# Kernel tuning notes

Hardware: AMD Instinct MI355X
Metric: run time of the kernel (lower is better)

Reference implementation:

```python
import jax, jax.numpy as jnp
import numpy as np

B, L, M = 8, 200, 4
S, D, Q = 100, 128, 10000
NRG = NPC = NAC = 20
F = 4                       # len(forget_window)+1
NTOT = F * (NRG + NPC + NAC + 15)   # 300


def setup_inputs():
    key = jax.random.key(0)
    ks = jax.random.split(key, 40)
    ri = lambda k, sh, hi: jax.random.randint(k, sh, 0, hi)
    rn = lambda k, sh: jax.random.normal(k, sh, jnp.float32) * 0.02

    def make_c(k1, k2):
        # distinct concept ids per (b,l) row (matches typical data; makes scatter deterministic)
        base = jax.random.randint(k1, (B, L, 1), 0, S)
        cc = (base + jnp.arange(M)) % S
        mask = jax.random.uniform(k2, (B, L, M)) < 0.2
        return jnp.where(mask, -1, cc)

    inp = dict(
        q=ri(ks[0], (B, L), Q),
        c=make_c(ks[1], ks[2]),
        shift_q=ri(ks[3], (B, L), Q),
        shift_c=make_c(ks[4], ks[5]),
        r=ri(ks[6], (B, L), 2),
        rgaps=ri(ks[7], (B, L, M), NRG),
        pcounts=ri(ks[8], (B, L, M, F), NPC),
        acounts=ri(ks[9], (B, L, M, F), NAC),
        shft_rgaps=ri(ks[10], (B, L, M), NRG),
        shft_pcounts=ri(ks[11], (B, L, M, F), NPC),
        shft_acounts=ri(ks[12], (B, L, M, F), NAC),
        E_skill=rn(ks[13], (S, D)),
        E_question=rn(ks[14], (Q, D)),
        E_response=rn(ks[15], (2, D)),
        wih_in=rn(ks[16], (4 * D, D)), whh_in=rn(ks[17], (4 * D, D)),
        bih_in=rn(ks[18], (4 * D,)), bhh_in=rn(ks[19], (4 * D,)),
        wih_fg=rn(ks[20], (4 * D, D)), whh_fg=rn(ks[21], (4 * D, D)),
        bih_fg=rn(ks[22], (4 * D,)), bhh_fg=rn(ks[23], (4 * D,)),
        W_l2=rn(ks[24], (3 * D, D)), b_l2=rn(ks[25], (D,)),
        W_l3=rn(ks[26], (2 * D, D)), b_l3=rn(ks[27], (D,)),
        W_fc3=rn(ks[28], (2 * D, 1)), b_fc3=rn(ks[29], (1,)),
        W_fc4=rn(ks[30], (2 * D, D)), b_fc4=rn(ks[31], (D,)),
        W_fc5=rn(ks[32], (2 * D, D)), b_fc5=rn(ks[33], (D,)),
        W_cemb=rn(ks[34], (NTOT, D)),                      # cemb, no bias
        W_pre=rn(ks[35], (S * (D + NTOT), D)), b_pre=rn(ks[36], (D,)),
    )
    return inp


def _lstm(x, wih, whh, bih, bhh):
    # Faithful to source: torch LSTM default is seq-first and the module passes
    # [B,L,D] unchanged, so recurrence runs over axis 0 of the given tensor.
    H = whh.shape[1]

    def step(carry, xt):
        h, cs = carry
        g = xt @ wih.T + h @ whh.T + bih + bhh
        i, f, gg, o = jnp.split(g, 4, axis=-1)
        cs = jax.nn.sigmoid(f) * cs + jax.nn.sigmoid(i) * jnp.tanh(gg)
        h = jax.nn.sigmoid(o) * jnp.tanh(cs)
        return (h, cs), h

    z = jnp.zeros((x.shape[1], H), x.dtype)
    _, hs = jax.lax.scan(step, (z, z), x)
    return hs


def _concept_true(c, E_skill):
    # eye(S+1)[c][..., :-1] summed over M: -1 maps to an all-zero row
    cv1 = jax.nn.one_hot(c, S).sum(-2)              # [B,L,S]
    return cv1[..., None] * E_skill[None, None]     # [B,L,S,D]


def _attention(q, ct):
    scores = jnp.einsum('bld,blsd->bls', q, ct) / jnp.asarray(np.sqrt(D), q.dtype)
    w = jax.nn.softmax(scores, axis=-1)
    return jnp.einsum('bls,blsd->bld', w, ct)


def _forget(c, rg, pc, ac, E_skill, W_cemb, W_pre, b_pre):
    rg4 = jnp.broadcast_to(rg[..., None], (B, L, M, F))
    fv1 = jnp.concatenate([
        jax.nn.one_hot(rg4, NRG + 5).reshape(B, L, M, -1),
        jax.nn.one_hot(pc, NPC + 5).reshape(B, L, M, -1),
        jax.nn.one_hot(ac, NAC + 5).reshape(B, L, M, -1)], -1)   # [B,L,M,NTOT]
    # vectorized masked scatter replacing the triple Python loop: -1 -> dummy row S
    tgt = jnp.where(c < 0, S, c)
    bi = jnp.arange(B)[:, None, None]
    li = jnp.arange(L)[None, :, None]
    fv2 = jnp.zeros((B, L, S + 1, NTOT), fv1.dtype).at[bi, li, tgt].set(fv1)[:, :, :S]
    Cct = fv2 @ W_cemb                                           # [B,L,S,D]
    theta = _concept_true(c, E_skill) * Cct
    theta = jnp.concatenate([theta, fv2], -1).reshape(B, L, -1)  # [B,L,S*(D+NTOT)]
    return theta @ W_pre + b_pre


def reference(q, c, shift_q, shift_c, r, rgaps, pcounts, acounts,
              shft_rgaps, shft_pcounts, shft_acounts,
              E_skill, E_question, E_response,
              wih_in, whh_in, bih_in, bhh_in,
              wih_fg, whh_fg, bih_fg, bhh_fg,
              W_l2, b_l2, W_l3, b_l3, W_fc3, b_fc3,
              W_fc4, b_fc4, W_fc5, b_fc5, W_cemb, W_pre, b_pre):
    emb_q = E_question[q]
    emb_r = E_response[r]
    att = _attention(emb_q, _concept_true(c, E_skill))
    xemb = jnp.concatenate([emb_q, emb_r, att], -1) @ W_l2 + b_l2
    input_h = _lstm(xemb, wih_in, whh_in, bih_in, bhh_in)        # dropout = eval identity
    fh = _forget(c, rgaps, pcounts, acounts, E_skill, W_cemb, W_pre, b_pre)
    forget_h = _lstm(fh, wih_fg, whh_fg, bih_fg, bhh_fg)
    shift = E_question[shift_q]
    s_att = _attention(shift, _concept_true(shift_c, E_skill))
    shift = jnp.concatenate([shift, s_att], -1) @ W_l3 + b_l3
    shift_forget = _forget(shift_c, shft_rgaps, shft_pcounts, shft_acounts,
                           E_skill, W_cemb, W_pre, b_pre)
    x1 = jax.nn.relu(jnp.concatenate([shift, input_h], -1) @ W_fc4 + b_fc4)
    x2 = jax.nn.relu(jnp.concatenate([shift_forget, forget_h], -1) @ W_fc5 + b_fc5)
    y = jax.nn.sigmoid(jnp.concatenate([x1, x2], -1) @ W_fc3 + b_fc3)
    return y.squeeze(-1)   # [B,L]
```

## Files before the change

kernel.cpp:

```cpp
#include <hip/hip_runtime.h>
#include <hip/hip_bf16.h>
#include <math.h>

#define BB   8
#define LL   200
#define MM   4
#define SS   100
#define DD   128
#define FF   4
#define NT   300
#define ROWS (BB*LL)
#define JT   32

#define NB_TR  128
#define NB_TP  1000
#define NB_AT  800
#define NB_PJ  400
#define NB_FH  1600

__device__ __forceinline__ float sigf(float x){ return 1.f/(1.f+expf(-x)); }

__global__ void __launch_bounds__(256) k_stage1(
    const float* __restrict__ wih_in, const float* __restrict__ wih_fg,
    const float* __restrict__ whh_in, const float* __restrict__ whh_fg,
    float* __restrict__ wT_in, float* __restrict__ wT_fg,
    float* __restrict__ whhT_in, float* __restrict__ whhT_fg,
    const float* __restrict__ Es, const float* __restrict__ Wc,
    const float* __restrict__ Wp, float* __restrict__ T,
    const int* __restrict__ q,  const int* __restrict__ c,
    const int* __restrict__ sq, const int* __restrict__ sc,
    const float* __restrict__ Eq,
    float* __restrict__ att0, float* __restrict__ att1)
{
    __shared__ float WcL[JT][128];
    int b   = blockIdx.x;
    int tid = threadIdx.x;

    if (b < NB_TR) {
        for (int e = b*256 + tid; e < 4*65536; e += NB_TR*256) {
            int mat = e >> 16, o = e & 65535;
            int k = o >> 9, g = o & 511;
            const float* src = (mat==0)?wih_in:(mat==1)?wih_fg:(mat==2)?whh_in:whh_fg;
            float*       dst = (mat==0)?wT_in:(mat==1)?wT_fg:(mat==2)?whhT_in:whhT_fg;
            dst[o] = src[g*128 + k];
        }
        return;
    }
    if (b < NB_TR + NB_TP) {
        int bb2 = b - NB_TR;
        int s  = bb2 / 10;
        int jc = bb2 - s*10;
        int j0 = jc * JT;
        const float* es = Es + s*128;
        for (int idx = tid; idx < JT*128; idx += 256) {
            int jj = idx >> 7, d = idx & 127;
            int j = j0 + jj;
            WcL[jj][d] = (j < NT) ? Wc[j*128 + d] * es[d] : 0.f;
        }
        __syncthreads();

        const float*  wp  = Wp + (size_t)s*428*128;
        const float2* wp2 = (const float2*)wp;
        int tt = tid & 63;
        int jg = tid >> 6;
        float2 acc[8];
        #pragma unroll
        for (int u = 0; u < 8; u++) acc[u] = make_float2(0.f, 0.f);
        for (int db = 0; db < 128; db += 8) {
            float2 wb[8];
            #pragma unroll
            for (int u = 0; u < 8; u++) wb[u] = wp2[(db+u)*64 + tt];
            #pragma unroll
            for (int u = 0; u < 8; u++) {
                #pragma unroll
                for (int j = 0; j < 8; j++) {
                    float wc = WcL[jg*8 + j][db + u];
                    acc[j].x += wc * wb[u].x;
                    acc[j].y += wc * wb[u].y;
                }
            }
        }
        const float2* wpe = (const float2*)(wp + 128*128);
        float2* T2 = (float2*)T;
        #pragma unroll
        for (int u = 0; u < 8; u++) {
            int j = j0 + jg*8 + u;
            if (j < NT) {
                float2 bv = wpe[(size_t)j*64 + tt];
                float2 o; o.x = acc[u].x + bv.x; o.y = acc[u].y + bv.y;
                T2[((size_t)s*NT + j)*64 + tt] = o;
            }
        }
        return;
    }
    {
        int wv   = tid >> 6;
        int lane = tid & 63;
        int task = (b - NB_TR - NB_TP)*4 + wv;
        int row   = task >> 1;
        int which = task & 1;
        const int* qq = which ? sq : q;
        const int* cc = which ? sc : c;
        float* out = which ? att1 : att0;

        size_t qb = (size_t)qq[row]*128;
        float eq0 = Eq[qb + lane];
        float eq1 = Eq[qb + 64 + lane];
        int   s[4];
        float es0[4], es1[4], d[4];
        #pragma unroll
        for (int m = 0; m < 4; m++) {
            s[m]  = cc[row*4 + m];
            es0[m] = (s[m] >= 0) ? Es[s[m]*128 + lane]      : 0.f;
            es1[m] = (s[m] >= 0) ? Es[s[m]*128 + 64 + lane] : 0.f;
            d[m] = eq0*es0[m] + eq1*es1[m];
        }
        #pragma unroll
        for (int off = 32; off > 0; off >>= 1) {
            #pragma unroll
            for (int m = 0; m < 4; m++) d[m] += __shfl_xor(d[m], off);
        }
        const float inv = 0.08838834764831845f;
        int   nact = 0;
        float mx = 0.f;
        #pragma unroll
        for (int m = 0; m < 4; m++) {
            d[m] *= inv;
            if (s[m] >= 0) { nact++; mx = fmaxf(mx, d[m]); }
        }
        float Z = (float)(SS - nact) * expf(-mx);
        float w[4];
        #pragma unroll
        for (int m = 0; m < 4; m++) {
            w[m] = (s[m] >= 0) ? expf(d[m] - mx) : 0.f;
            Z += w[m];
        }
        float a0 = 0.f, a1 = 0.f;
        #pragma unroll
        for (int m = 0; m < 4; m++) {
            float ww = w[m]/Z;
            a0 += ww * es0[m];
            a1 += ww * es1[m];
        }
        out[row*128 + lane]      = a0;
        out[row*128 + 64 + lane] = a1;
    }
}

__global__ void __launch_bounds__(256) k_stage2(
    const int* __restrict__ q, const int* __restrict__ r, const int* __restrict__ sq,
    const float* __restrict__ Eq, const float* __restrict__ Er,
    const float* __restrict__ att, const float* __restrict__ satt,
    const float* __restrict__ Wl2, const float* __restrict__ bl2,
    const float* __restrict__ Wl3, const float* __restrict__ bl3,
    float* __restrict__ xemb, float* __restrict__ shiftx,
    const int* __restrict__ c,  const int* __restrict__ rg,
    const int* __restrict__ pc, const int* __restrict__ ac,
    const int* __restrict__ sc, const int* __restrict__ srg,
    const int* __restrict__ spc,const int* __restrict__ sac,
    const float* __restrict__ T, const float* __restrict__ bpre,
    float* __restrict__ fh0, float* __restrict__ fh1)
{
    __shared__ float xs1[4][384];
    __shared__ float xs2[4][256];
    __shared__ float part[2][4][128];
    int b   = blockIdx.x;
    int tid = threadIdx.x;

    if (b < NB_PJ) {
        int r0 = b*4;
        for (int e = tid; e < 4*384; e += 256) {
            int i = e / 384, pos = e - i*384;
            int row = r0 + i;
            float v;
            if (pos < 128)      v = Eq[(size_t)q[row]*128 + pos];
            else if (pos < 256) v = Er[r[row]*128 + (pos-128)];
            else                v = att[row*128 + (pos-256)];
            xs1[i][pos] = v;
        }
        for (int e = tid; e < 4*256; e += 256) {
            int i = e >> 8, pos = e & 255;
            int row = r0 + i;
            xs2[i][pos] = (pos < 128) ? Eq[(size_t)sq[row]*128 + pos]
                                      : satt[row*128 + (pos-128)];
        }
        __syncthreads();

        int kg  = tid >> 7;
        int col = tid & 127;
        {
            float acc[4];
            #pragma unroll
            for (int i = 0; i < 4; i++) acc[i] = 0.f;
            int k0 = kg*192;
            for (int kb = 0; kb < 192; kb += 8) {
                float wb[8];
                #pragma unroll
                for (int u = 0; u < 8; u++) wb[u] = Wl2[(k0+kb+u)*128 + col];
                #pragma unroll
                for (int u = 0; u < 8; u++) {
                    #pragma unroll
                    for (int i = 0; i < 4; i++) acc[i] += xs1[i][k0+kb+u]*wb[u];
                }
            }
            #pragma unroll
            for (int i = 0; i < 4; i++) part[kg][i][col] = acc[i];
        }
        __syncthreads();
        for (int e = tid; e < 512; e += 256) {
            int i = e >> 7, cc2 = e & 127;
            xemb[(r0+i)*128 + cc2] = bl2[cc2] + part[0][i][cc2] + part[1][i][cc2];
        }
        __syncthreads();
        {
            float acc[4];
            #pragma unroll
            for (int i = 0; i < 4; i++) acc[i] = 0.f;
            int k0 = kg*128;
            for (int kb = 0; kb < 128; kb += 8) {
                float wb[8];
                #pragma unroll
                for (int u = 0; u < 8; u++) wb[u] = Wl3[(k0+kb+u)*128 + col];
                #pragma unroll
                for (int u = 0; u < 8; u++) {
                    #pragma unroll
                    for (int i = 0; i < 4; i++) acc[i] += xs2[i][k0+kb+u]*wb[u];
                }
            }
            #pragma unroll
            for (int i = 0; i < 4; i++) part[kg][i][col] = acc[i];
        }
        __syncthreads();
        for (int e = tid; e < 512; e += 256) {
            int i = e >> 7, cc2 = e & 127;
            shiftx[(r0+i)*128 + cc2] = bl3[cc2] + part[0][i][cc2] + part[1][i][cc2];
        }
        return;
    }
    {
        int u     = (b - NB_PJ)*2 + (tid >> 7);
        int which = u & 1;
        int row   = u >> 1;
        int t     = tid & 127;
        const int* C  = which ? sc  : c;
        const int* RG = which ? srg : rg;
        const int* PC = which ? spc : pc;
        const int* AC = which ? sac : ac;
        float* out = which ? fh1 : fh0;

        float acc = bpre[t];
        for (int m = 0; m < 4; m++) {
            int s = C[row*4 + m];
            if (s < 0) continue;
            int rgv = RG[row*4 + m];
            const float* Ts = T + (size_t)s*NT*128;
            #pragma unroll
            for (int f = 0; f < 4; f++) {
                int j1 = f*25 + rgv;
                int j2 = 100 + f*25 + PC[(row*4+m)*4 + f];
                int j3 = 200 + f*25 + AC[(row*4+m)*4 + f];
                acc += Ts[j1*128 + t] + Ts[j2*128 + t] + Ts[j3*128 + t];
            }
        }
        out[row*128 + t] = acc;
    }
}

__global__ void __launch_bounds__(512) k_lstm(
    const float* __restrict__ xemb, const float* __restrict__ fh,
    const float* __restrict__ wT_in, const float* __restrict__ wT_fg,
    const float* __restrict__ whhT_in, const float* __restrict__ whhT_fg,
    const float* __restrict__ bih_in, const float* __restrict__ bhh_in,
    const float* __restrict__ bih_fg, const float* __restrict__ bhh_fg,
    float* __restrict__ h_in_out, float* __restrict__ h_fg_out)
{
    int which = blockIdx.y;
    const float* X  = which ? fh      : xemb;
    const float* WI = which ? wT_fg   : wT_in;
    const float* WH = which ? whhT_fg : whhT_in;
    const float* B1 = which ? bih_fg  : bih_in;
    const float* B2 = which ? bhh_fg  : bhh_in;
    float* OUT = which ? h_fg_out : h_in_out;

    int l0  = blockIdx.x * 2;
    int tid = threadIdx.x;

    __shared__ float xr[16][128];
    __shared__ float gb[16][512];
    __shared__ float h[2][128], cs[2][128], gl[2][512];

    for (int e = tid; e < 2048; e += 512) {
        int i = e >> 7, d = e & 127;
        int t = i >> 1, rr = i & 1;
        xr[i][d] = X[(size_t)(t*200 + l0 + rr)*128 + d];
    }
    if (tid < 256) { h[tid>>7][tid&127] = 0.f; cs[tid>>7][tid&127] = 0.f; }
    __syncthreads();

    float bb = B1[tid] + B2[tid];
    {
        float a[16];
        #pragma unroll
        for (int i = 0; i < 16; i++) a[i] = bb;
        for (int kb = 0; kb < 128; kb += 8) {
            float wv[8];
            #pragma unroll
            for (int u = 0; u < 8; u++) wv[u] = WI[(kb+u)*512 + tid];
            #pragma unroll
            for (int u = 0; u < 8; u++) {
                #pragma unroll
                for (int i = 0; i < 16; i++) a[i] += xr[i][kb+u]*wv[u];
            }
        }
        #pragma unroll
        for (int i = 0; i < 16; i++) gb[i][tid] = a[i];
    }

    float w[128];
    #pragma unroll
    for (int k = 0; k < 128; k++) w[k] = WH[k*512 + tid];
    __syncthreads();

    for (int t = 0; t < 8; t++) {
        float a0 = gb[t*2 + 0][tid];
        float a1 = gb[t*2 + 1][tid];
        #pragma unroll
        for (int k = 0; k < 128; k++) {
            float h0 = h[0][k], h1 = h[1][k];
            a0 += h0*w[k];
            a1 += h1*w[k];
        }
        gl[0][tid] = a0;
        gl[1][tid] = a1;
        __syncthreads();
        if (tid < 256) {
            int rr = tid >> 7, d = tid & 127;
            float gi = gl[rr][d], gf = gl[rr][128+d], gg = gl[rr][256+d], go = gl[rr][384+d];
            float cn = sigf(gf)*cs[rr][d] + sigf(gi)*tanhf(gg);
            float hn = sigf(go)*tanhf(cn);
            cs[rr][d] = cn;
            h[rr][d]  = hn;
            OUT[(size_t)(t*200 + l0 + rr)*128 + d] = hn;
        }
        __syncthreads();
    }
}

__global__ void __launch_bounds__(256) k_final(
    const float* __restrict__ shiftx, const float* __restrict__ h_in,
    const float* __restrict__ fh_shift, const float* __restrict__ h_fg,
    const float* __restrict__ Wfc4, const float* __restrict__ bfc4,
    const float* __restrict__ Wfc5, const float* __restrict__ bfc5,
    const float* __restrict__ Wfc3, const float* __restrict__ bfc3,
    float* __restrict__ out)
{
    int r0  = blockIdx.x * 4;
    int tid = threadIdx.x;
    int kg  = tid >> 7;
    int col = tid & 127;
    __shared__ float xa[4][256], xb[4][256];
    __shared__ float part[2][4][128];

    for (int e = tid; e < 4*256; e += 256) {
        int i = e >> 8, pos = e & 255;
        int row = r0 + i;
        xa[i][pos] = (pos < 128) ? shiftx[row*128 + pos]   : h_in[row*128 + pos-128];
        xb[i][pos] = (pos < 128) ? fh_shift[row*128 + pos] : h_fg[row*128 + pos-128];
    }
    __syncthreads();

    float acc4[4], acc5[4];
    #pragma unroll
    for (int i = 0; i < 4; i++) { acc4[i] = 0.f; acc5[i] = 0.f; }
    int k0 = kg * 128;
    for (int kb = 0; kb < 128; kb += 8) {
        float w4[8], w5[8];
        #pragma unroll
        for (int u = 0; u < 8; u++) {
            w4[u] = Wfc4[(k0+kb+u)*128 + col];
            w5[u] = Wfc5[(k0+kb+u)*128 + col];
        }
        #pragma unroll
        for (int u = 0; u < 8; u++) {
            int k = k0 + kb + u;
            #pragma unroll
            for (int i = 0; i < 4; i++) {
                acc4[i] += xa[i][k] * w4[u];
                acc5[i] += xb[i][k] * w5[u];
            }
        }
    }

    #pragma unroll
    for (int i = 0; i < 4; i++) part[kg][i][col] = acc4[i];
    __syncthreads();
    float x1r[2];
    #pragma unroll
    for (int j = 0; j < 2; j++) {
        int e = tid + 256*j;
        int i = e >> 7, cc2 = e & 127;
        x1r[j] = fmaxf(part[0][i][cc2] + part[1][i][cc2] + bfc4[cc2], 0.f);
    }
    __syncthreads();
    #pragma unroll
    for (int i = 0; i < 4; i++) part[kg][i][col] = acc5[i];
    __syncthreads();
    float x2r[2];
    #pragma unroll
    for (int j = 0; j < 2; j++) {
        int e = tid + 256*j;
        int i = e >> 7, cc2 = e & 127;
        x2r[j] = fmaxf(part[0][i][cc2] + part[1][i][cc2] + bfc5[cc2], 0.f);
    }
    __syncthreads();

    float* cont = &part[0][0][0];
    #pragma unroll
    for (int j = 0; j < 2; j++) {
        int e = tid + 256*j;
        int i = e >> 7, cc2 = e & 127;
        cont[i*128 + cc2] = x1r[j]*Wfc3[cc2] + x2r[j]*Wfc3[128 + cc2];
    }
    __syncthreads();
    int wv = tid >> 6, lane = tid & 63;
    float sum = cont[wv*128 + lane] + cont[wv*128 + lane + 64];
    #pragma unroll
    for (int off = 32; off > 0; off >>= 1) sum += __shfl_xor(sum, off);
    if (lane == 0) out[r0 + wv] = 1.f/(1.f + expf(-(sum + bfc3[0])));
}

extern "C" void kernel_launch(void* const* d_in, const int* in_sizes, int n_in,
                              void* d_out, int out_size, void* d_ws, size_t ws_size,
                              hipStream_t stream)
{
    const int*   q      = (const int*)d_in[0];
    const int*   c      = (const int*)d_in[1];
    const int*   sq     = (const int*)d_in[2];
    const int*   sc     = (const int*)d_in[3];
    const int*   r      = (const int*)d_in[4];
    const int*   rg     = (const int*)d_in[5];
    const int*   pc     = (const int*)d_in[6];
    const int*   ac     = (const int*)d_in[7];
    const int*   srg    = (const int*)d_in[8];
    const int*   spc    = (const int*)d_in[9];
    const int*   sac    = (const int*)d_in[10];
    const float* Es     = (const float*)d_in[11];
    const float* Eq     = (const float*)d_in[12];
    const float* Er     = (const float*)d_in[13];
    const float* wih_in = (const float*)d_in[14];
    const float* whh_in = (const float*)d_in[15];
    const float* bih_in = (const float*)d_in[16];
    const float* bhh_in = (const float*)d_in[17];
    const float* wih_fg = (const float*)d_in[18];
    const float* whh_fg = (const float*)d_in[19];
    const float* bih_fg = (const float*)d_in[20];
    const float* bhh_fg = (const float*)d_in[21];
    const float* Wl2    = (const float*)d_in[22];
    const float* bl2    = (const float*)d_in[23];
    const float* Wl3    = (const float*)d_in[24];
    const float* bl3    = (const float*)d_in[25];
    const float* Wfc3   = (const float*)d_in[26];
    const float* bfc3   = (const float*)d_in[27];
    const float* Wfc4   = (const float*)d_in[28];
    const float* bfc4   = (const float*)d_in[29];
    const float* Wfc5   = (const float*)d_in[30];
    const float* bfc5   = (const float*)d_in[31];
    const float* Wc     = (const float*)d_in[32];
    const float* Wp     = (const float*)d_in[33];
    const float* bpre   = (const float*)d_in[34];

    float* W = (float*)d_ws;
    float* T       = W;  W += 100*NT*128;
    float* att     = W;  W += ROWS*128;
    float* satt    = W;  W += ROWS*128;
    float* xemb    = W;  W += ROWS*128;
    float* shiftx  = W;  W += ROWS*128;
    float* fh0     = W;  W += ROWS*128;
    float* fh1     = W;  W += ROWS*128;
    float* wT_in   = W;  W += 512*128;
    float* wT_fg   = W;  W += 512*128;
    float* whhT_in = W;  W += 512*128;
    float* whhT_fg = W;  W += 512*128;
    float* h_in    = W;  W += ROWS*128;
    float* h_fg    = W;  W += ROWS*128;

    hipLaunchKernelGGL(k_stage1, dim3(NB_TR + NB_TP + NB_AT), dim3(256), 0, stream,
        wih_in, wih_fg, whh_in, whh_fg, wT_in, wT_fg, whhT_in, whhT_fg,
        Es, Wc, Wp, T,
        q, c, sq, sc, Eq, att, satt);

    hipLaunchKernelGGL(k_stage2, dim3(NB_PJ + NB_FH), dim3(256), 0, stream,
        q, r, sq, Eq, Er, att, satt, Wl2, bl2, Wl3, bl3, xemb, shiftx,
        c, rg, pc, ac, sc, srg, spc, sac, T, bpre, fh0, fh1);

    hipLaunchKernelGGL(k_lstm, dim3(100, 2), dim3(512), 0, stream,
        xemb, fh0, wT_in, wT_fg, whhT_in, whhT_fg,
        bih_in, bhh_in, bih_fg, bhh_fg, h_in, h_fg);

    hipLaunchKernelGGL(k_final, dim3(400), dim3(256), 0, stream,
        shiftx, h_in, fh1, h_fg, Wfc4, bfc4, Wfc5, bfc5, Wfc3, bfc3, (float*)d_out);
}
```

Baseline: 232.5 us.

## Store forget table in bf16, widen T-projection tiles, one LSTM column per block

The precomputed forget table T is now written and read as bf16, halving its memory footprint and the gather traffic in stage 2. The T-projection blocks now compute 64 output rows each with float4 accumulators (half as many blocks). The LSTM kernel processes one sequence column per block instead of two, doubling the grid to 400 blocks to shorten each block's work. The bf16 storage adds rounding error to the forget path, and each LSTM block now reloads the full recurrent weight set to serve a single column.

```diff
diff --git a/kernel.cpp b/kernel.cpp
--- a/kernel.cpp
+++ b/kernel.cpp
@@ -10,15 +10,24 @@
 #define FF   4
 #define NT   300
 #define ROWS (BB*LL)
-#define JT   32
+#define JT2  64
 
 #define NB_TR  128
-#define NB_TP  1000
+#define NB_TP  500
 #define NB_AT  800
 #define NB_PJ  400
 #define NB_FH  1600
 
 __device__ __forceinline__ float sigf(float x){ return 1.f/(1.f+expf(-x)); }
+
+__device__ __forceinline__ unsigned short f2bf(float x){
+    unsigned int u = __float_as_uint(x);
+    unsigned int r = (u + 0x7FFFu + ((u >> 16) & 1u)) >> 16;
+    return (unsigned short)r;
+}
+__device__ __forceinline__ float bf2f(unsigned short v){
+    return __uint_as_float(((unsigned int)v) << 16);
+}
 
 __global__ void __launch_bounds__(256) k_stage1(
     const float* __restrict__ wih_in, const float* __restrict__ wih_fg,
@@ -26,13 +35,13 @@
     float* __restrict__ wT_in, float* __restrict__ wT_fg,
     float* __restrict__ whhT_in, float* __restrict__ whhT_fg,
     const float* __restrict__ Es, const float* __restrict__ Wc,
-    const float* __restrict__ Wp, float* __restrict__ T,
+    const float* __restrict__ Wp, unsigned short* __restrict__ T16,
     const int* __restrict__ q,  const int* __restrict__ c,
     const int* __restrict__ sq, const int* __restrict__ sc,
     const float* __restrict__ Eq,
     float* __restrict__ att0, float* __restrict__ att1)
 {
-    __shared__ float WcL[JT][128];
+    __shared__ float WcL[JT2][128];
     int b   = blockIdx.x;
     int tid = threadIdx.x;
 
@@ -48,11 +57,11 @@
     }
     if (b < NB_TR + NB_TP) {
         int bb2 = b - NB_TR;
-        int s  = bb2 / 10;
-        int jc = bb2 - s*10;
-        int j0 = jc * JT;
+        int s  = bb2 / 5;
+        int jc = bb2 - s*5;
+        int j0 = jc * JT2;
         const float* es = Es + s*128;
-        for (int idx = tid; idx < JT*128; idx += 256) {
+        for (int idx = tid; idx < JT2*128; idx += 256) {
             int jj = idx >> 7, d = idx & 127;
             int j = j0 + jj;
             WcL[jj][d] = (j < NT) ? Wc[j*128 + d] * es[d] : 0.f;
@@ -60,35 +69,48 @@
         __syncthreads();
 
         const float*  wp  = Wp + (size_t)s*428*128;
-        const float2* wp2 = (const float2*)wp;
-        int tt = tid & 63;
-        int jg = tid >> 6;
-        float2 acc[8];
-        #pragma unroll
-        for (int u = 0; u < 8; u++) acc[u] = make_float2(0.f, 0.f);
-        for (int db = 0; db < 128; db += 8) {
-            float2 wb[8];
-            #pragma unroll
-            for (int u = 0; u < 8; u++) wb[u] = wp2[(db+u)*64 + tt];
-            #pragma unroll
-            for (int u = 0; u < 8; u++) {
+        const float4* wp4 = (const float4*)wp;
+        int tq = tid & 31;
+        int jg = tid >> 5;
+        float4 acc[8];
+        #pragma unroll
+        for (int j = 0; j < 8; j++) acc[j] = make_float4(0.f,0.f,0.f,0.f);
+
+        for (int d4 = 0; d4 < 128; d4 += 4) {
+            float4 wv[4];
+            #pragma unroll
+            for (int u = 0; u < 4; u++) wv[u] = wp4[(d4+u)*32 + tq];
+            float4 wc[8];
+            #pragma unroll
+            for (int j = 0; j < 8; j++)
+                wc[j] = *(const float4*)&WcL[jg*8 + j][d4];
+            #pragma unroll
+            for (int u = 0; u < 4; u++) {
+                float4 wpv = wv[u];
                 #pragma unroll
                 for (int j = 0; j < 8; j++) {
-                    float wc = WcL[jg*8 + j][db + u];
-                    acc[j].x += wc * wb[u].x;
-                    acc[j].y += wc * wb[u].y;
+                    float w = (u==0)?wc[j].x:(u==1)?wc[j].y:(u==2)?wc[j].z:wc[j].w;
+                    acc[j].x += w * wpv.x;
+                    acc[j].y += w * wpv.y;
+                    acc[j].z += w * wpv.z;
+                    acc[j].w += w * wpv.w;
                 }
             }
         }
-        const float2* wpe = (const float2*)(wp + 128*128);
-        float2* T2 = (float2*)T;
-        #pragma unroll
-        for (int u = 0; u < 8; u++) {
-            int j = j0 + jg*8 + u;
-            if (j < NT) {
-                float2 bv = wpe[(size_t)j*64 + tt];
-                float2 o; o.x = acc[u].x + bv.x; o.y = acc[u].y + bv.y;
-                T2[((size_t)s*NT + j)*64 + tt] = o;
+
+        const float4* wpe4 = (const float4*)(wp + 128*128);
+        ushort4* T4 = (ushort4*)T16;
+        #pragma unroll
+        for (int j = 0; j < 8; j++) {
+            int jj = j0 + jg*8 + j;
+            if (jj < NT) {
+                float4 bv = wpe4[(size_t)jj*32 + tq];
+                ushort4 st;
+                st.x = f2bf(acc[j].x + bv.x);
+                st.y = f2bf(acc[j].y + bv.y);
+                st.z = f2bf(acc[j].z + bv.z);
+                st.w = f2bf(acc[j].w + bv.w);
+                T4[((size_t)s*NT + jj)*32 + tq] = st;
             }
         }
         return;
@@ -158,7 +180,7 @@
     const int* __restrict__ pc, const int* __restrict__ ac,
     const int* __restrict__ sc, const int* __restrict__ srg,
     const int* __restrict__ spc,const int* __restrict__ sac,
-    const float* __restrict__ T, const float* __restrict__ bpre,
+    const unsigned short* __restrict__ T16, const float* __restrict__ bpre,
     float* __restrict__ fh0, float* __restrict__ fh1)
 {
     __shared__ float xs1[4][384];
@@ -253,13 +275,13 @@
             int s = C[row*4 + m];
             if (s < 0) continue;
             int rgv = RG[row*4 + m];
-            const float* Ts = T + (size_t)s*NT*128;
+            const unsigned short* Ts = T16 + (size_t)s*NT*128;
             #pragma unroll
             for (int f = 0; f < 4; f++) {
                 int j1 = f*25 + rgv;
                 int j2 = 100 + f*25 + PC[(row*4+m)*4 + f];
                 int j3 = 200 + f*25 + AC[(row*4+m)*4 + f];
-                acc += Ts[j1*128 + t] + Ts[j2*128 + t] + Ts[j3*128 + t];
+                acc += bf2f(Ts[j1*128 + t]) + bf2f(Ts[j2*128 + t]) + bf2f(Ts[j3*128 + t]);
             }
         }
         out[row*128 + t] = acc;
@@ -282,26 +304,25 @@
     const float* B2 = which ? bhh_fg  : bhh_in;
     float* OUT = which ? h_fg_out : h_in_out;
 
-    int l0  = blockIdx.x * 2;
+    int l0  = blockIdx.x;
     int tid = threadIdx.x;
 
-    __shared__ float xr[16][128];
-    __shared__ float gb[16][512];
-    __shared__ float h[2][128], cs[2][128], gl[2][512];
-
-    for (int e = tid; e < 2048; e += 512) {
-        int i = e >> 7, d = e & 127;
-        int t = i >> 1, rr = i & 1;
-        xr[i][d] = X[(size_t)(t*200 + l0 + rr)*128 + d];
-    }
-    if (tid < 256) { h[tid>>7][tid&127] = 0.f; cs[tid>>7][tid&127] = 0.f; }
+    __shared__ float xr[8][128];
+    __shared__ float gb[8][512];
+    __shared__ float h[128], cs[128], gl[512];
+
+    for (int e = tid; e < 1024; e += 512) {
+        int t = e >> 7, d = e & 127;
+        xr[t][d] = X[(size_t)(t*200 + l0)*128 + d];
+    }
+    if (tid < 128) { h[tid] = 0.f; cs[tid] = 0.f; }
     __syncthreads();
 
     float bb = B1[tid] + B2[tid];
     {
-        float a[16];
-        #pragma unroll
-        for (int i = 0; i < 16; i++) a[i] = bb;
+        float a[8];
+        #pragma unroll
+        for (int i = 0; i < 8; i++) a[i] = bb;
         for (int kb = 0; kb < 128; kb += 8) {
             float wv[8];
             #pragma unroll
@@ -309,11 +330,11 @@
             #pragma unroll
             for (int u = 0; u < 8; u++) {
                 #pragma unroll
-                for (int i = 0; i < 16; i++) a[i] += xr[i][kb+u]*wv[u];
-            }
-        }
-        #pragma unroll
-        for (int i = 0; i < 16; i++) gb[i][tid] = a[i];
+                for (int i = 0; i < 8; i++) a[i] += xr[i][kb+u]*wv[u];
+            }
+        }
+        #pragma unroll
+        for (int i = 0; i < 8; i++) gb[i][tid] = a[i];
     }
 
     float w[128];
@@ -322,25 +343,18 @@
     __syncthreads();
 
     for (int t = 0; t < 8; t++) {
-        float a0 = gb[t*2 + 0][tid];
-        float a1 = gb[t*2 + 1][tid];
-        #pragma unroll
-        for (int k = 0; k < 128; k++) {
-            float h0 = h[0][k], h1 = h[1][k];
-            a0 += h0*w[k];
-            a1 += h1*w[k];
-        }
-        gl[0][tid] = a0;
-        gl[1][tid] = a1;
-        __syncthreads();
-        if (tid < 256) {
-            int rr = tid >> 7, d = tid & 127;
-            float gi = gl[rr][d], gf = gl[rr][128+d], gg = gl[rr][256+d], go = gl[rr][384+d];
-            float cn = sigf(gf)*cs[rr][d] + sigf(gi)*tanhf(gg);
+        float a0 = gb[t][tid];
+        #pragma unroll
+        for (int k = 0; k < 128; k++) a0 += h[k]*w[k];
+        gl[tid] = a0;
+        __syncthreads();
+        if (tid < 128) {
+            float gi = gl[tid], gf = gl[128+tid], gg = gl[256+tid], go = gl[384+tid];
+            float cn = sigf(gf)*cs[tid] + sigf(gi)*tanhf(gg);
             float hn = sigf(go)*tanhf(cn);
-            cs[rr][d] = cn;
-            h[rr][d]  = hn;
-            OUT[(size_t)(t*200 + l0 + rr)*128 + d] = hn;
+            cs[tid] = cn;
+            h[tid]  = hn;
+            OUT[(size_t)(t*200 + l0)*128 + tid] = hn;
         }
         __syncthreads();
     }
@@ -470,7 +484,7 @@
     const float* bpre   = (const float*)d_in[34];
 
     float* W = (float*)d_ws;
-    float* T       = W;  W += 100*NT*128;
+    unsigned short* T16 = (unsigned short*)W;  W += 100*NT*128/2;
     float* att     = W;  W += ROWS*128;
     float* satt    = W;  W += ROWS*128;
     float* xemb    = W;  W += ROWS*128;
@@ -486,14 +500,14 @@
 
     hipLaunchKernelGGL(k_stage1, dim3(NB_TR + NB_TP + NB_AT), dim3(256), 0, stream,
         wih_in, wih_fg, whh_in, whh_fg, wT_in, wT_fg, whhT_in, whhT_fg,
-        Es, Wc, Wp, T,
+        Es, Wc, Wp, T16,
         q, c, sq, sc, Eq, att, satt);
 
     hipLaunchKernelGGL(k_stage2, dim3(NB_PJ + NB_FH), dim3(256), 0, stream,
         q, r, sq, Eq, Er, att, satt, Wl2, bl2, Wl3, bl3, xemb, shiftx,
-        c, rg, pc, ac, sc, srg, spc, sac, T, bpre, fh0, fh1);
-
-    hipLaunchKernelGGL(k_lstm, dim3(100, 2), dim3(512), 0, stream,
+        c, rg, pc, ac, sc, srg, spc, sac, T16, bpre, fh0, fh1);
+
+    hipLaunchKernelGGL(k_lstm, dim3(200, 2), dim3(512), 0, stream,
         xemb, fh0, wT_in, wT_fg, whhT_in, whhT_fg,
         bih_in, bhh_in, bih_fg, bhh_fg, h_in, h_fg);
 
```

New measurement: 246.1 us. 5.8% more time.
